# Kernel optimization log

Measured on AMD Instinct MI355X. Metric: run time of the kernel, lower is better.

## Reference

```python
import jax, jax.numpy as jnp
import numpy as np

FP8_MAX = 448.0  # float8_e4m3fn max normal
BLOCK = 128

def quant_dequant(x, block_size=BLOCK):
    """Block-wise fp8 (e4m3) activation/kernel quantization along last dim,
    immediately dequantized (mathematically equivalent to fp8 GEMM with
    per-block scales applied during accumulation)."""
    *lead, d = x.shape
    xb = x.reshape(*lead, d // block_size, block_size)
    scale = jnp.max(jnp.abs(xb), axis=-1, keepdims=True) / FP8_MAX
    scale = jnp.maximum(scale, 1e-12)
    q = (xb / scale).astype(jnp.float8_e4m3fn).astype(x.dtype)
    return (q * scale).reshape(x.shape)

def fp8_linear(x, W, b, block_size=BLOCK):
    y = jnp.dot(quant_dequant(x, block_size), quant_dequant(W, block_size))
    return y + b

def setup_inputs() -> dict:
    key = jax.random.key(0)
    ks = jax.random.split(key, 3)
    B, S, D = 2, 2048, 1024
    x = jax.random.normal(ks[0], (B, S, D), dtype=jnp.float32)
    W_qkv = jax.random.normal(ks[1], (D, 3 * D), dtype=jnp.float32) * (1.0 / np.sqrt(D))
    b_qkv = jnp.zeros((3 * D,), dtype=jnp.float32)
    W_out = jax.random.normal(ks[2], (D, D), dtype=jnp.float32) * (1.0 / np.sqrt(D))
    b_out = jnp.zeros((D,), dtype=jnp.float32)
    return {"x": x, "W_qkv": W_qkv, "b_qkv": b_qkv, "W_out": W_out, "b_out": b_out}

def reference(x, W_qkv, b_qkv, W_out, b_out):
    NUM_HEADS, HEAD_DIM = 16, 64
    B, S, _ = x.shape
    # fp8-quantized QKV projection
    qkv = fp8_linear(x, W_qkv, b_qkv)                       # [B,S,3*H*Dh]
    qkv = qkv.reshape(B, S, 3, NUM_HEADS, HEAD_DIM).transpose(2, 0, 3, 1, 4)
    q, k, v = qkv[0], qkv[1], qkv[2]                        # each [B,H,S,Dh]
    scale = 1.0 / jnp.sqrt(jnp.float32(HEAD_DIM)).astype(x.dtype)
    attn = jnp.einsum('bhqd,bhkd->bhqk', q, k) * scale      # [B,H,S,S]
    attn = jax.nn.softmax(attn, axis=-1)
    out = jnp.einsum('bhqk,bhkd->bhqd', attn, v)            # [B,H,S,Dh]
    out = out.transpose(0, 2, 1, 3).reshape(B, S, NUM_HEADS * HEAD_DIM)
    # fp8-quantized output projection; present (kv cache) is None here
    return fp8_linear(out, W_out, b_out)
```

## Files before the change

### kernel.cpp

```cpp
#include <hip/hip_runtime.h>
#include <cstdint>
#include <cstddef>

typedef __attribute__((ext_vector_type(8))) short bfrag;
typedef __attribute__((ext_vector_type(8))) _Float16 hfrag;
typedef __attribute__((ext_vector_type(2))) __fp16 fp16x2;
typedef __attribute__((ext_vector_type(4))) float f4;
typedef __attribute__((ext_vector_type(16))) float f16v;

#define MFMA16H(a, b, c) __builtin_amdgcn_mfma_f32_16x16x32_f16(a, b, c, 0, 0, 0)
#define MFMA32H(a, b, c) __builtin_amdgcn_mfma_f32_32x32x16_f16(a, b, c, 0, 0, 0)

__device__ __forceinline__ unsigned cvt_pkrtz_u(float a, float b) {
  union { fp16x2 h; unsigned u; } c;
  c.h = __builtin_amdgcn_cvt_pkrtz(a, b);
  return c.u;
}
__device__ __forceinline__ unsigned short f2h_bits(float x) {
  _Float16 h = (_Float16)x;
  union { _Float16 h; unsigned short u; } c;
  c.h = h;
  return c.u;
}
__device__ __forceinline__ void permswap(unsigned& a, unsigned& b) {
  auto r = __builtin_amdgcn_permlane32_swap((int)a, (int)b, false, false);
  a = (unsigned)r[0];
  b = (unsigned)r[1];
}
__device__ __forceinline__ void gl16(const unsigned short* g, unsigned short* l) {
  __builtin_amdgcn_global_load_lds(
      (const __attribute__((address_space(1))) unsigned int*)g,
      (__attribute__((address_space(3))) unsigned int*)l, 16, 0, 0);
}

__device__ __forceinline__ float qd_e4m3(float v) {
  float a = fabsf(v);
  unsigned u = __float_as_uint(a);
  int e = (int)(u >> 23) - 127;
  int k = e - 3;
  if (k < -9) k = -9;
  float big = __uint_as_float((unsigned)(k + 150) << 23);
  float r = (a + big) - big;
  return __builtin_copysignf(r, v);
}

__global__ __launch_bounds__(256) void quant_x(const float* __restrict__ src,
                                               unsigned short* __restrict__ q,
                                               float* __restrict__ s,
                                               int nblk) {
  int gid = blockIdx.x * 256 + threadIdx.x;
  int wid = gid >> 6;
  int lane = gid & 63;
  if (wid >= nblk) return;
  size_t off = (size_t)wid * 128 + lane * 2;
  float2 xv = *reinterpret_cast<const float2*>(src + off);
  float m = fmaxf(fabsf(xv.x), fabsf(xv.y));
#pragma unroll
  for (int d = 32; d > 0; d >>= 1) m = fmaxf(m, __shfl_xor(m, d));
  float scale = fmaxf(m / 448.0f, 1e-12f);
  unsigned short q0 = f2h_bits(qd_e4m3(xv.x / scale));
  unsigned short q1 = f2h_bits(qd_e4m3(xv.y / scale));
  *reinterpret_cast<unsigned*>(q + off) = (unsigned)q0 | ((unsigned)q1 << 16);
  if (lane == 0) s[wid] = scale;
}

__global__ __launch_bounds__(256) void quant_w_t(const float* __restrict__ W,
                                                 unsigned short* __restrict__ WT,
                                                 int K, int N) {
  __shared__ __align__(16) unsigned short Ht[128][72];
  const int tid = threadIdx.x;
  const int w = tid >> 6, l = tid & 63;
  const int k0 = blockIdx.y * 64, n0 = blockIdx.x * 128;
#pragma unroll 4
  for (int i = 0; i < 16; ++i) {
    int kl = w * 16 + i;
    float2 xv = *reinterpret_cast<const float2*>(&W[(size_t)(k0 + kl) * N + n0 + l * 2]);
    float m = fmaxf(fabsf(xv.x), fabsf(xv.y));
#pragma unroll
    for (int d = 32; d > 0; d >>= 1) m = fmaxf(m, __shfl_xor(m, d));
    float scale = fmaxf(m / 448.0f, 1e-12f);
    Ht[l * 2][kl]     = f2h_bits(qd_e4m3(xv.x / scale) * scale);
    Ht[l * 2 + 1][kl] = f2h_bits(qd_e4m3(xv.y / scale) * scale);
  }
  __syncthreads();
  const int n = tid & 127, hs = tid >> 7;
  unsigned short* dst = WT + (size_t)(n0 + n) * K + k0 + hs * 32;
#pragma unroll
  for (int j = 0; j < 4; ++j)
    *reinterpret_cast<bfrag*>(dst + j * 8) =
        *reinterpret_cast<const bfrag*>(&Ht[n][hs * 32 + j * 8]);
}

template <int MF, bool SPLIT>
__global__ __launch_bounds__(256, 2) void gemm_q(const unsigned short* __restrict__ Aq,
                                                 const float* __restrict__ As,
                                                 const unsigned short* __restrict__ WT,
                                                 const float* __restrict__ bias,
                                                 float* __restrict__ Cf,
                                                 unsigned short* __restrict__ C16,
                                                 int M, int N, int K) {
  constexpr int MT = MF * 32;
  __shared__ __align__(16) unsigned short Al[MT][64];
  __shared__ __align__(16) unsigned short Bh[128][64];
  __shared__ float Ss[MT][8];
  const int tid = threadIdx.x;
  const int w = tid >> 6, l = tid & 63;
  const int lr = l & 15, lg = l >> 4;
  const int nbx = N >> 7;
  const int nwg = nbx * (M / MT);
  const int q8 = nwg >> 3;
  const int swz = ((int)blockIdx.x & 7) * q8 + ((int)blockIdx.x >> 3);
  const int row0 = (swz / nbx) * MT, col0 = (swz % nbx) << 7;
  const int wr = (w >> 1) * (MT / 2), wc = (w & 1) * 64;
  const int xsw = (lr & 7) * 8;

  if (MF == 4) {
    int r = tid >> 1, c0 = (tid & 1) * 4;
    *reinterpret_cast<float4*>(&Ss[r][c0]) =
        *reinterpret_cast<const float4*>(&As[(size_t)(row0 + r) * 8 + c0]);
  } else {
    int r = tid >> 2, c0 = (tid & 3) * 2;
    *reinterpret_cast<float2*>(&Ss[r][c0]) =
        *reinterpret_cast<const float2*>(&As[(size_t)(row0 + r) * 8 + c0]);
  }

  f4 acc[MF][4], seg[MF][4];
#pragma unroll
  for (int i = 0; i < MF; ++i)
#pragma unroll
    for (int j = 0; j < 4; ++j)
#pragma unroll
      for (int c = 0; c < 4; ++c) {
        acc[i][j][c] = 0.f;
        seg[i][j][c] = 0.f;
      }

  const int lrow = l >> 3;
  const int jch = (l & 7) ^ lrow;
  const unsigned short* pA = Aq + (size_t)(row0 + w * (MT / 4) + lrow) * K + jch * 8;
  const unsigned short* pH = WT + (size_t)(col0 + w * 32 + lrow) * K + jch * 8;
  unsigned short* dA = &Al[0][0] + w * (MT / 4) * 64;
  unsigned short* dH = &Bh[0][0] + w * 2048;

  const int niter = K >> 6;
  for (int it = 0; it < niter; ++it) {
    const int k0 = it << 6;
    __syncthreads();
#pragma unroll
    for (int ii = 0; ii < MF; ++ii)
      gl16(pA + (size_t)ii * 8 * K + k0, dA + ii * 512);
#pragma unroll
    for (int ii = 0; ii < 4; ++ii)
      gl16(pH + (size_t)ii * 8 * K + k0, dH + ii * 512);
    __syncthreads();

#pragma unroll
    for (int ks = 0; ks < 2; ++ks) {
      hfrag af[MF];
#pragma unroll
      for (int mf = 0; mf < MF; ++mf)
        af[mf] = *reinterpret_cast<const hfrag*>(
            &Al[0][0] + (wr + mf * 16 + lr) * 64 + ((ks * 32 + lg * 8) ^ xsw));
#pragma unroll
      for (int nf = 0; nf < 4; ++nf) {
        hfrag bh = *reinterpret_cast<const hfrag*>(
            &Bh[0][0] + (wc + nf * 16 + lr) * 64 + ((ks * 32 + lg * 8) ^ xsw));
#pragma unroll
        for (int mf = 0; mf < MF; ++mf)
          seg[mf][nf] = MFMA16H(af[mf], bh, seg[mf][nf]);
      }
    }

    if (it & 1) {
      const int kb = it >> 1;
#pragma unroll
      for (int mf = 0; mf < MF; ++mf) {
        float sv[4];
#pragma unroll
        for (int r = 0; r < 4; ++r) sv[r] = Ss[wr + mf * 16 + lg * 4 + r][kb];
#pragma unroll
        for (int nf = 0; nf < 4; ++nf)
#pragma unroll
          for (int r = 0; r < 4; ++r) {
            acc[mf][nf][r] += sv[r] * seg[mf][nf][r];
            seg[mf][nf][r] = 0.f;
          }
      }
    }
  }

#pragma unroll
  for (int mf = 0; mf < MF; ++mf) {
#pragma unroll
    for (int r = 0; r < 4; ++r) {
      const int m = row0 + wr + mf * 16 + lg * 4 + r;
#pragma unroll
      for (int nf = 0; nf < 4; ++nf) {
        const int col = col0 + wc + nf * 16 + lr;
        float o = acc[mf][nf][r] + bias[col];
        if (SPLIT) {
          C16[(size_t)m * N + col] = f2h_bits(o);
        } else {
          Cf[(size_t)m * N + col] = o;
        }
      }
    }
  }
}

__global__ __launch_bounds__(256, 2) void attn_mfma32(const unsigned short* __restrict__ qkv,
                                                      float* __restrict__ out) {
  __shared__ __align__(16) unsigned short Vth[2][64][40];
  const int tid = threadIdx.x;
  const int w = tid >> 6, l = tid & 63;
  const int q = l & 31;
  const int hi = l >> 5;
  const int lin = (int)blockIdx.x;
  const int xcd = lin & 7, j = lin >> 3;
  const int bh = 4 * xcd + (j >> 4);
  const int qt = j & 15;
  const int q0 = qt * 128 + w * 32;
  const int b = bh >> 4, h = bh & 15;
  const size_t bbase = (size_t)b * 2048;
  const size_t hoff = (size_t)h * 64;

  const int rA = (q & 24) | ((q + (q >> 3)) & 7);
  const int rB = 32 + ((q & 24) | ((q + 4 + (q >> 3)) & 7));

  hfrag qh[4];
  {
    const size_t qrow = (bbase + q0 + q) * 3072 + hoff + hi * 8;
#pragma unroll
    for (int f = 0; f < 4; ++f)
      qh[f] = *reinterpret_cast<const hfrag*>(qkv + qrow + f * 16);
  }

  const int skp = tid >> 3;
  const int sc = tid & 7;

  const unsigned short* kph = qkv + (bbase + q) * 3072 + 1024 + hoff + hi * 8;
  const unsigned short* vph = qkv + (bbase + skp) * 3072 + 2048 + hoff + sc * 8;
  const size_t KSTEP = (size_t)32 * 3072;

  hfrag kh[4];
  bfrag svh;

#pragma unroll
  for (int f = 0; f < 4; ++f)
    kh[f] = *reinterpret_cast<const hfrag*>(kph + f * 16);
  svh = *reinterpret_cast<const bfrag*>(vph);
  vph += KSTEP;
#pragma unroll
  for (int j2 = 0; j2 < 8; ++j2) {
    int row = sc * 8 + ((j2 + sc) & 7);
    Vth[0][row][skp] = (unsigned short)svh[j2];
  }
  f16v sA, sB;
#pragma unroll
  for (int r = 0; r < 16; ++r) sA[r] = 0.f;
  __builtin_amdgcn_s_setprio(1);
#pragma unroll
  for (int f = 0; f < 4; ++f) sA = MFMA32H(kh[f], qh[f], sA);
  __builtin_amdgcn_s_setprio(0);
  kph += KSTEP;
#pragma unroll
  for (int f = 0; f < 4; ++f)
    kh[f] = *reinterpret_cast<const hfrag*>(kph + f * 16);
  __syncthreads();

  f16v oA0, oA1;
#pragma unroll
  for (int r = 0; r < 16; ++r) { oA0[r] = 0.f; oA1[r] = 0.f; }
  float m_i = -1e30f, l_i = 0.f;

#define ATTN_ITER(KT, SCUR, SNXT)                                              \
  do {                                                                         \
    const int kt_ = (KT);                                                      \
    const int cur_ = kt_ & 1;                                                  \
         \
    if (kt_ < 63) {                                                            \
      _Pragma("unroll") for (int r = 0; r < 16; ++r) SNXT[r] = 0.f;            \
      __builtin_amdgcn_s_setprio(1);                                           \
      _Pragma("unroll") for (int f = 0; f < 4; ++f)                            \
          SNXT = MFMA32H(kh[f], qh[f], SNXT);                                  \
      __builtin_amdgcn_s_setprio(0);                                           \
    }                                                                          \
                                                         \
    if (kt_ < 62) {                                                            \
      kph += KSTEP;                                                            \
      _Pragma("unroll") for (int f = 0; f < 4; ++f)                            \
          kh[f] = *reinterpret_cast<const hfrag*>(kph + f * 16);               \
    }                                                                          \
                        \
    float a0 = fmaxf(SCUR[0], SCUR[1]), a1 = fmaxf(SCUR[2], SCUR[3]);          \
    float a2 = fmaxf(SCUR[4], SCUR[5]), a3 = fmaxf(SCUR[6], SCUR[7]);          \
    float a4 = fmaxf(SCUR[8], SCUR[9]), a5 = fmaxf(SCUR[10], SCUR[11]);        \
    float a6 = fmaxf(SCUR[12], SCUR[13]), a7 = fmaxf(SCUR[14], SCUR[15]);      \
    float b0_ = fmaxf(a0, a1), b1_ = fmaxf(a2, a3);                            \
    float b2_ = fmaxf(a4, a5), b3_ = fmaxf(a6, a7);                            \
    float mt = fmaxf(fmaxf(b0_, b1_), fmaxf(b2_, b3_));                        \
    mt = fmaxf(mt, __shfl_xor(mt, 32));                                        \
    mt *= 0.125f;                                                              \
    if (!__all(mt <= m_i)) {                \
      float mn = fmaxf(m_i, mt);                                               \
      float corr = __expf(m_i - mn);                                           \
      m_i = mn;                                                                \
      l_i *= corr;                                                             \
      _Pragma("unroll") for (int r = 0; r < 16; ++r) {                         \
        oA0[r] *= corr; oA1[r] *= corr;                                        \
      }                                                                        \
    }                                                                          \
    float p[16];                                                               \
    _Pragma("unroll") for (int r = 0; r < 16; ++r)                             \
        p[r] = __expf(fmaf(SCUR[r], 0.125f, -m_i));                            \
    float r0_ = (p[0] + p[1]) + (p[2] + p[3]);                                 \
    float r1_ = (p[4] + p[5]) + (p[6] + p[7]);                                 \
    float r2_ = (p[8] + p[9]) + (p[10] + p[11]);                               \
    float r3_ = (p[12] + p[13]) + (p[14] + p[15]);                             \
    float rs = (r0_ + r1_) + (r2_ + r3_);                                      \
    rs += __shfl_xor(rs, 32);                                                  \
    l_i += rs;                                                                 \
                         \
    if (kt_ < 63) {                                                            \
      svh = *reinterpret_cast<const bfrag*>(vph);                              \
      vph += KSTEP;                                                            \
    }                                                                          \
                       \
    unsigned ph_[8];                                                           \
    _Pragma("unroll") for (int i = 0; i < 8; ++i)                              \
        ph_[i] = cvt_pkrtz_u(p[2 * i], p[2 * i + 1]);                          \
    permswap(ph_[0], ph_[2]); permswap(ph_[1], ph_[3]);                        \
    permswap(ph_[4], ph_[6]); permswap(ph_[5], ph_[7]);                        \
    union U4 { unsigned u[4]; hfrag f; };                                      \
    U4 f0h, f1h;                                                               \
    f0h.u[0] = ph_[0]; f0h.u[1] = ph_[1]; f0h.u[2] = ph_[2]; f0h.u[3] = ph_[3];\
    f1h.u[0] = ph_[4]; f1h.u[1] = ph_[5]; f1h.u[2] = ph_[6]; f1h.u[3] = ph_[7];\
                         \
    __builtin_amdgcn_s_setprio(1);                                             \
    _Pragma("unroll") for (int c = 0; c < 2; ++c) {                            \
      hfrag pF = c ? f1h.f : f0h.f;                                            \
      hfrag vh0 = *reinterpret_cast<const hfrag*>(&Vth[cur_][rA][c * 16 + hi * 8]); \
      hfrag vh1 = *reinterpret_cast<const hfrag*>(&Vth[cur_][rB][c * 16 + hi * 8]); \
      oA0 = MFMA32H(vh0, pF, oA0);                                             \
      oA1 = MFMA32H(vh1, pF, oA1);                                             \
    }                                                                          \
    __builtin_amdgcn_s_setprio(0);                                             \
              \
    if (kt_ < 63) {                                                            \
      _Pragma("unroll") for (int j2 = 0; j2 < 8; ++j2) {                       \
        int row = sc * 8 + ((j2 + sc) & 7);                                    \
        Vth[cur_ ^ 1][row][skp] = (unsigned short)svh[j2];                     \
      }                                                                        \
      __syncthreads();                                                         \
    }                                                                          \
  } while (0)

  for (int kt = 0; kt < 64; kt += 2) {
    ATTN_ITER(kt, sA, sB);
    ATTN_ITER(kt + 1, sB, sA);
  }
#undef ATTN_ITER

  float inv = 1.0f / l_i;
  const size_t orow = (bbase + q0 + q) * 1024 + hoff;
#pragma unroll
  for (int dblk = 0; dblk < 2; ++dblk) {
#pragma unroll
    for (int rg = 0; rg < 4; ++rg) {
      float4 o;
      if (dblk == 0) {
        o.x = oA0[rg * 4 + 0] * inv;
        o.y = oA0[rg * 4 + 1] * inv;
        o.z = oA0[rg * 4 + 2] * inv;
        o.w = oA0[rg * 4 + 3] * inv;
      } else {
        o.x = oA1[rg * 4 + 0] * inv;
        o.y = oA1[rg * 4 + 1] * inv;
        o.z = oA1[rg * 4 + 2] * inv;
        o.w = oA1[rg * 4 + 3] * inv;
      }
      *reinterpret_cast<float4*>(out + orow + dblk * 32 + rg * 8 + hi * 4) = o;
    }
  }
}

extern "C" void kernel_launch(void* const* d_in, const int* in_sizes, int n_in,
                              void* d_out, int out_size, void* d_ws, size_t ws_size,
                              hipStream_t stream) {
  const float* x     = (const float*)d_in[0];
  const float* W_qkv = (const float*)d_in[1];
  const float* b_qkv = (const float*)d_in[2];
  const float* W_out = (const float*)d_in[3];
  const float* b_out = (const float*)d_in[4];
  float* y = (float*)d_out;

  char* ws = (char*)d_ws;
  const size_t MB = 1u << 20;
  unsigned short* x_q   = (unsigned short*)(ws);
  float*          s_x   = (float*)(ws + 8 * MB);
  unsigned short* wqh   = (unsigned short*)(ws + 8 * MB + 256 * 1024);
  unsigned short* woh   = (unsigned short*)(ws + 20 * MB + 256 * 1024);
  unsigned short* qkv   = (unsigned short*)(ws + 24 * MB + 256 * 1024);

  quant_x<<<8192, 256, 0, stream>>>(x, x_q, s_x, 32768);
  quant_w_t<<<dim3(24, 16), 256, 0, stream>>>(W_qkv, wqh, 1024, 3072);
  quant_w_t<<<dim3(8, 16), 256, 0, stream>>>(W_out, woh, 1024, 1024);

  gemm_q<4, true><<<768, 256, 0, stream>>>(x_q, s_x, wqh, b_qkv,
                                           nullptr, qkv, 4096, 3072, 1024);

  attn_mfma32<<<512, 256, 0, stream>>>(qkv, y);

  quant_x<<<8192, 256, 0, stream>>>(y, x_q, s_x, 32768);

  gemm_q<2, false><<<512, 256, 0, stream>>>(x_q, s_x, woh, b_out,
                                            y, nullptr, 4096, 1024, 1024);
}
```

Baseline: 177.4 us.

## Split attention KV range into two halves and merge partials in combine kernel

Attention now runs as a split-KV (flash-decoding style) computation. Each block handles half of the key/value sequence, so the grid doubles to 1024 blocks, and the launch bound rises to 4 blocks per SM. Each block writes its unnormalized partial output plus its running max and sum. A new combine kernel rescales and merges the two halves. The goal is more parallelism and occupancy on the GPU. In exchange it adds an extra 16MB fp32 partial write and read, a second launch, and drops the software-pipelined S computation, which may expose MFMA and load latency.

```diff
diff --git a/kernel.cpp b/kernel.cpp
--- a/kernel.cpp
+++ b/kernel.cpp
@@ -208,8 +208,10 @@
   }
 }
 
-__global__ __launch_bounds__(256, 2) void attn_mfma32(const unsigned short* __restrict__ qkv,
-                                                      float* __restrict__ out) {
+__global__ __launch_bounds__(256, 4) void attn_mfma32(const unsigned short* __restrict__ qkv,
+                                                      float* __restrict__ O0,
+                                                      float* __restrict__ O1,
+                                                      float2* __restrict__ ml) {
   __shared__ __align__(16) unsigned short Vth[2][64][40];
   const int tid = threadIdx.x;
   const int w = tid >> 6, l = tid & 63;
@@ -217,11 +219,13 @@
   const int hi = l >> 5;
   const int lin = (int)blockIdx.x;
   const int xcd = lin & 7, j = lin >> 3;
-  const int bh = 4 * xcd + (j >> 4);
-  const int qt = j & 15;
+  const int bh = 4 * xcd + (j >> 5);
+  const int qt = (j & 31) >> 1;
+  const int half = j & 1;
   const int q0 = qt * 128 + w * 32;
   const int b = bh >> 4, h = bh & 15;
   const size_t bbase = (size_t)b * 2048;
+  const size_t kvbase = bbase + (size_t)half * 1024;
   const size_t hoff = (size_t)h * 64;
 
   const int rA = (q & 24) | ((q + (q >> 3)) & 7);
@@ -238,8 +242,8 @@
   const int skp = tid >> 3;
   const int sc = tid & 7;
 
-  const unsigned short* kph = qkv + (bbase + q) * 3072 + 1024 + hoff + hi * 8;
-  const unsigned short* vph = qkv + (bbase + skp) * 3072 + 2048 + hoff + sc * 8;
+  const unsigned short* kph = qkv + (kvbase + q) * 3072 + 1024 + hoff + hi * 8;
+  const unsigned short* vph = qkv + (kvbase + skp) * 3072 + 2048 + hoff + sc * 8;
   const size_t KSTEP = (size_t)32 * 3072;
 
   hfrag kh[4];
@@ -255,17 +259,6 @@
     int row = sc * 8 + ((j2 + sc) & 7);
     Vth[0][row][skp] = (unsigned short)svh[j2];
   }
-  f16v sA, sB;
-#pragma unroll
-  for (int r = 0; r < 16; ++r) sA[r] = 0.f;
-  __builtin_amdgcn_s_setprio(1);
-#pragma unroll
-  for (int f = 0; f < 4; ++f) sA = MFMA32H(kh[f], qh[f], sA);
-  __builtin_amdgcn_s_setprio(0);
-  kph += KSTEP;
-#pragma unroll
-  for (int f = 0; f < 4; ++f)
-    kh[f] = *reinterpret_cast<const hfrag*>(kph + f * 16);
   __syncthreads();
 
   f16v oA0, oA1;
@@ -273,115 +266,129 @@
   for (int r = 0; r < 16; ++r) { oA0[r] = 0.f; oA1[r] = 0.f; }
   float m_i = -1e30f, l_i = 0.f;
 
-#define ATTN_ITER(KT, SCUR, SNXT)                                              \
-  do {                                                                         \
-    const int kt_ = (KT);                                                      \
-    const int cur_ = kt_ & 1;                                                  \
-         \
-    if (kt_ < 63) {                                                            \
-      _Pragma("unroll") for (int r = 0; r < 16; ++r) SNXT[r] = 0.f;            \
-      __builtin_amdgcn_s_setprio(1);                                           \
-      _Pragma("unroll") for (int f = 0; f < 4; ++f)                            \
-          SNXT = MFMA32H(kh[f], qh[f], SNXT);                                  \
-      __builtin_amdgcn_s_setprio(0);                                           \
-    }                                                                          \
-                                                         \
-    if (kt_ < 62) {                                                            \
-      kph += KSTEP;                                                            \
-      _Pragma("unroll") for (int f = 0; f < 4; ++f)                            \
-          kh[f] = *reinterpret_cast<const hfrag*>(kph + f * 16);               \
-    }                                                                          \
-                        \
-    float a0 = fmaxf(SCUR[0], SCUR[1]), a1 = fmaxf(SCUR[2], SCUR[3]);          \
-    float a2 = fmaxf(SCUR[4], SCUR[5]), a3 = fmaxf(SCUR[6], SCUR[7]);          \
-    float a4 = fmaxf(SCUR[8], SCUR[9]), a5 = fmaxf(SCUR[10], SCUR[11]);        \
-    float a6 = fmaxf(SCUR[12], SCUR[13]), a7 = fmaxf(SCUR[14], SCUR[15]);      \
-    float b0_ = fmaxf(a0, a1), b1_ = fmaxf(a2, a3);                            \
-    float b2_ = fmaxf(a4, a5), b3_ = fmaxf(a6, a7);                            \
-    float mt = fmaxf(fmaxf(b0_, b1_), fmaxf(b2_, b3_));                        \
-    mt = fmaxf(mt, __shfl_xor(mt, 32));                                        \
-    mt *= 0.125f;                                                              \
-    if (!__all(mt <= m_i)) {                \
-      float mn = fmaxf(m_i, mt);                                               \
-      float corr = __expf(m_i - mn);                                           \
-      m_i = mn;                                                                \
-      l_i *= corr;                                                             \
-      _Pragma("unroll") for (int r = 0; r < 16; ++r) {                         \
-        oA0[r] *= corr; oA1[r] *= corr;                                        \
-      }                                                                        \
-    }                                                                          \
-    float p[16];                                                               \
-    _Pragma("unroll") for (int r = 0; r < 16; ++r)                             \
-        p[r] = __expf(fmaf(SCUR[r], 0.125f, -m_i));                            \
-    float r0_ = (p[0] + p[1]) + (p[2] + p[3]);                                 \
-    float r1_ = (p[4] + p[5]) + (p[6] + p[7]);                                 \
-    float r2_ = (p[8] + p[9]) + (p[10] + p[11]);                               \
-    float r3_ = (p[12] + p[13]) + (p[14] + p[15]);                             \
-    float rs = (r0_ + r1_) + (r2_ + r3_);                                      \
-    rs += __shfl_xor(rs, 32);                                                  \
-    l_i += rs;                                                                 \
-                         \
-    if (kt_ < 63) {                                                            \
-      svh = *reinterpret_cast<const bfrag*>(vph);                              \
-      vph += KSTEP;                                                            \
-    }                                                                          \
-                       \
-    unsigned ph_[8];                                                           \
-    _Pragma("unroll") for (int i = 0; i < 8; ++i)                              \
-        ph_[i] = cvt_pkrtz_u(p[2 * i], p[2 * i + 1]);                          \
-    permswap(ph_[0], ph_[2]); permswap(ph_[1], ph_[3]);                        \
-    permswap(ph_[4], ph_[6]); permswap(ph_[5], ph_[7]);                        \
-    union U4 { unsigned u[4]; hfrag f; };                                      \
-    U4 f0h, f1h;                                                               \
-    f0h.u[0] = ph_[0]; f0h.u[1] = ph_[1]; f0h.u[2] = ph_[2]; f0h.u[3] = ph_[3];\
-    f1h.u[0] = ph_[4]; f1h.u[1] = ph_[5]; f1h.u[2] = ph_[6]; f1h.u[3] = ph_[7];\
-                         \
-    __builtin_amdgcn_s_setprio(1);                                             \
-    _Pragma("unroll") for (int c = 0; c < 2; ++c) {                            \
-      hfrag pF = c ? f1h.f : f0h.f;                                            \
-      hfrag vh0 = *reinterpret_cast<const hfrag*>(&Vth[cur_][rA][c * 16 + hi * 8]); \
-      hfrag vh1 = *reinterpret_cast<const hfrag*>(&Vth[cur_][rB][c * 16 + hi * 8]); \
-      oA0 = MFMA32H(vh0, pF, oA0);                                             \
-      oA1 = MFMA32H(vh1, pF, oA1);                                             \
-    }                                                                          \
-    __builtin_amdgcn_s_setprio(0);                                             \
-              \
-    if (kt_ < 63) {                                                            \
-      _Pragma("unroll") for (int j2 = 0; j2 < 8; ++j2) {                       \
-        int row = sc * 8 + ((j2 + sc) & 7);                                    \
-        Vth[cur_ ^ 1][row][skp] = (unsigned short)svh[j2];                     \
-      }                                                                        \
-      __syncthreads();                                                         \
-    }                                                                          \
-  } while (0)
-
-  for (int kt = 0; kt < 64; kt += 2) {
-    ATTN_ITER(kt, sA, sB);
-    ATTN_ITER(kt + 1, sB, sA);
-  }
-#undef ATTN_ITER
-
-  float inv = 1.0f / l_i;
-  const size_t orow = (bbase + q0 + q) * 1024 + hoff;
+  for (int kt = 0; kt < 32; ++kt) {
+    const int cur = kt & 1;
+
+    f16v S;
+#pragma unroll
+    for (int r = 0; r < 16; ++r) S[r] = 0.f;
+    __builtin_amdgcn_s_setprio(1);
+#pragma unroll
+    for (int f = 0; f < 4; ++f) S = MFMA32H(kh[f], qh[f], S);
+    __builtin_amdgcn_s_setprio(0);
+
+    if (kt < 31) {
+      kph += KSTEP;
+#pragma unroll
+      for (int f = 0; f < 4; ++f)
+        kh[f] = *reinterpret_cast<const hfrag*>(kph + f * 16);
+    }
+
+    float a0 = fmaxf(S[0], S[1]), a1 = fmaxf(S[2], S[3]);
+    float a2 = fmaxf(S[4], S[5]), a3 = fmaxf(S[6], S[7]);
+    float a4 = fmaxf(S[8], S[9]), a5 = fmaxf(S[10], S[11]);
+    float a6 = fmaxf(S[12], S[13]), a7 = fmaxf(S[14], S[15]);
+    float b0_ = fmaxf(a0, a1), b1_ = fmaxf(a2, a3);
+    float b2_ = fmaxf(a4, a5), b3_ = fmaxf(a6, a7);
+    float mt = fmaxf(fmaxf(b0_, b1_), fmaxf(b2_, b3_));
+    mt = fmaxf(mt, __shfl_xor(mt, 32));
+    mt *= 0.125f;
+    if (!__all(mt <= m_i)) {
+      float mn = fmaxf(m_i, mt);
+      float corr = __expf(m_i - mn);
+      m_i = mn;
+      l_i *= corr;
+#pragma unroll
+      for (int r = 0; r < 16; ++r) { oA0[r] *= corr; oA1[r] *= corr; }
+    }
+    float p[16];
+#pragma unroll
+    for (int r = 0; r < 16; ++r) p[r] = __expf(fmaf(S[r], 0.125f, -m_i));
+    float r0_ = (p[0] + p[1]) + (p[2] + p[3]);
+    float r1_ = (p[4] + p[5]) + (p[6] + p[7]);
+    float r2_ = (p[8] + p[9]) + (p[10] + p[11]);
+    float r3_ = (p[12] + p[13]) + (p[14] + p[15]);
+    float rs = (r0_ + r1_) + (r2_ + r3_);
+    rs += __shfl_xor(rs, 32);
+    l_i += rs;
+
+    if (kt < 31) {
+      svh = *reinterpret_cast<const bfrag*>(vph);
+      vph += KSTEP;
+    }
+
+    unsigned ph_[8];
+#pragma unroll
+    for (int i = 0; i < 8; ++i)
+      ph_[i] = cvt_pkrtz_u(p[2 * i], p[2 * i + 1]);
+    permswap(ph_[0], ph_[2]); permswap(ph_[1], ph_[3]);
+    permswap(ph_[4], ph_[6]); permswap(ph_[5], ph_[7]);
+    union U4 { unsigned u[4]; hfrag f; };
+    U4 f0h, f1h;
+    f0h.u[0] = ph_[0]; f0h.u[1] = ph_[1]; f0h.u[2] = ph_[2]; f0h.u[3] = ph_[3];
+    f1h.u[0] = ph_[4]; f1h.u[1] = ph_[5]; f1h.u[2] = ph_[6]; f1h.u[3] = ph_[7];
+
+    __builtin_amdgcn_s_setprio(1);
+#pragma unroll
+    for (int c = 0; c < 2; ++c) {
+      hfrag pF = c ? f1h.f : f0h.f;
+      hfrag vh0 = *reinterpret_cast<const hfrag*>(&Vth[cur][rA][c * 16 + hi * 8]);
+      hfrag vh1 = *reinterpret_cast<const hfrag*>(&Vth[cur][rB][c * 16 + hi * 8]);
+      oA0 = MFMA32H(vh0, pF, oA0);
+      oA1 = MFMA32H(vh1, pF, oA1);
+    }
+    __builtin_amdgcn_s_setprio(0);
+
+    if (kt < 31) {
+#pragma unroll
+      for (int j2 = 0; j2 < 8; ++j2) {
+        int row = sc * 8 + ((j2 + sc) & 7);
+        Vth[cur ^ 1][row][skp] = (unsigned short)svh[j2];
+      }
+      __syncthreads();
+    }
+  }
+
+  float* dst = half ? O1 : O0;
+  const size_t row = bbase + q0 + q;
+  const size_t orow = row * 1024 + hoff;
 #pragma unroll
   for (int dblk = 0; dblk < 2; ++dblk) {
 #pragma unroll
     for (int rg = 0; rg < 4; ++rg) {
       float4 o;
       if (dblk == 0) {
-        o.x = oA0[rg * 4 + 0] * inv;
-        o.y = oA0[rg * 4 + 1] * inv;
-        o.z = oA0[rg * 4 + 2] * inv;
-        o.w = oA0[rg * 4 + 3] * inv;
+        o.x = oA0[rg * 4 + 0]; o.y = oA0[rg * 4 + 1];
+        o.z = oA0[rg * 4 + 2]; o.w = oA0[rg * 4 + 3];
       } else {
-        o.x = oA1[rg * 4 + 0] * inv;
-        o.y = oA1[rg * 4 + 1] * inv;
-        o.z = oA1[rg * 4 + 2] * inv;
-        o.w = oA1[rg * 4 + 3] * inv;
-      }
-      *reinterpret_cast<float4*>(out + orow + dblk * 32 + rg * 8 + hi * 4) = o;
-    }
-  }
+        o.x = oA1[rg * 4 + 0]; o.y = oA1[rg * 4 + 1];
+        o.z = oA1[rg * 4 + 2]; o.w = oA1[rg * 4 + 3];
+      }
+      *reinterpret_cast<float4*>(dst + orow + dblk * 32 + rg * 8 + hi * 4) = o;
+    }
+  }
+  if (hi == 0) ml[(size_t)half * (4096 * 16) + row * 16 + h] = make_float2(m_i, l_i);
+}
+
+__global__ __launch_bounds__(256) void attn_combine(float* __restrict__ O0,
+                                                    const float* __restrict__ O1,
+                                                    const float2* __restrict__ ml) {
+  int gid = blockIdx.x * 256 + threadIdx.x;
+  int row = gid >> 8;
+  int h = (gid & 255) >> 4;
+  float2 ml0 = ml[(size_t)row * 16 + h];
+  float2 ml1 = ml[(size_t)(4096 * 16) + (size_t)row * 16 + h];
+  float m = fmaxf(ml0.x, ml1.x);
+  float a0 = __expf(ml0.x - m), a1 = __expf(ml1.x - m);
+  float inv = 1.0f / fmaf(ml0.y, a0, ml1.y * a1);
+  float4 o0 = reinterpret_cast<const float4*>(O0)[gid];
+  float4 o1 = reinterpret_cast<const float4*>(O1)[gid];
+  float4 o;
+  o.x = fmaf(o0.x, a0, o1.x * a1) * inv;
+  o.y = fmaf(o0.y, a0, o1.y * a1) * inv;
+  o.z = fmaf(o0.z, a0, o1.z * a1) * inv;
+  o.w = fmaf(o0.w, a0, o1.w * a1) * inv;
+  reinterpret_cast<float4*>(O0)[gid] = o;
 }
 
 extern "C" void kernel_launch(void* const* d_in, const int* in_sizes, int n_in,
@@ -401,6 +408,8 @@
   unsigned short* wqh   = (unsigned short*)(ws + 8 * MB + 256 * 1024);
   unsigned short* woh   = (unsigned short*)(ws + 20 * MB + 256 * 1024);
   unsigned short* qkv   = (unsigned short*)(ws + 24 * MB + 256 * 1024);
+  float*          O1    = (float*)(ws + 48 * MB + 256 * 1024);
+  float2*         ml    = (float2*)(ws + 64 * MB + 256 * 1024);
 
   quant_x<<<8192, 256, 0, stream>>>(x, x_q, s_x, 32768);
   quant_w_t<<<dim3(24, 16), 256, 0, stream>>>(W_qkv, wqh, 1024, 3072);
@@ -409,7 +418,8 @@
   gemm_q<4, true><<<768, 256, 0, stream>>>(x_q, s_x, wqh, b_qkv,
                                            nullptr, qkv, 4096, 3072, 1024);
 
-  attn_mfma32<<<512, 256, 0, stream>>>(qkv, y);
+  attn_mfma32<<<1024, 256, 0, stream>>>(qkv, y, O1, ml);
+  attn_combine<<<4096, 256, 0, stream>>>(y, O1, ml);
 
   quant_x<<<8192, 256, 0, stream>>>(y, x_q, s_x, 32768);
 
```

Result: slower. 184.1 us (+3.8%).
